# Optimization experiments

Hardware: AMD Instinct MI355X
Metric: run time of the kernel (lower is better)

Reference implementation:

```python
import jax, jax.numpy as jnp
import numpy as np

B, S, V, D, H, NL, FF, MAXD, OUTLEN, NC = 8, 1024, 64, 512, 8, 6, 2048, 64, 8, 10
HD = D // H


def _layernorm(x, g, b, eps=1e-5):
    m = jnp.mean(x, axis=-1, keepdims=True)
    v = jnp.var(x, axis=-1, keepdims=True)
    return (x - m) * jax.lax.rsqrt(v + eps) * g + b


def setup_inputs() -> dict:
    key = jax.random.key(0)
    ks = jax.random.split(key, 24)
    s = 0.02
    inp = {
        'src': jax.random.randint(ks[0], (B, S), 0, V, dtype=jnp.int32),
        'src_pad_mask': jnp.zeros((B, S), dtype=bool),
        'embed': jax.random.normal(ks[1], (V, D), jnp.float32) * s,
        'cls_token': jnp.zeros((D,), jnp.float32),
        'qkv_w': jax.random.normal(ks[2], (NL, 3 * D, D), jnp.float32) * s,
        'qkv_b': jnp.zeros((NL, 3 * D), jnp.float32),
        'out_w': jax.random.normal(ks[3], (NL, D, D), jnp.float32) * s,
        'out_b': jnp.zeros((NL, D), jnp.float32),
        'rel_emb': jax.random.normal(ks[4], (NL, 2 * MAXD + 1, H), jnp.float32) * s,
        'ln1_g': jnp.ones((NL, D), jnp.float32),
        'ln1_b': jnp.zeros((NL, D), jnp.float32),
        'w1': jax.random.normal(ks[5], (NL, FF, D), jnp.float32) * s,
        'b1': jnp.zeros((NL, FF), jnp.float32),
        'w2': jax.random.normal(ks[6], (NL, D, FF), jnp.float32) * s,
        'b2': jnp.zeros((NL, D), jnp.float32),
        'ln2_g': jnp.ones((NL, D), jnp.float32),
        'ln2_b': jnp.zeros((NL, D), jnp.float32),
        'norm_g': jnp.ones((D,), jnp.float32),
        'norm_b': jnp.zeros((D,), jnp.float32),
        'cls_w': jax.random.normal(ks[7], (OUTLEN * NC, D), jnp.float32) * s,
        'cls_b': jnp.zeros((OUTLEN * NC,), jnp.float32),
    }
    return inp


def _forward(src, src_pad_mask, embed, cls_token, qkv_w, qkv_b, out_w, out_b,
             rel_emb, ln1_g, ln1_b, w1, b1, w2, b2, ln2_g, ln2_b,
             norm_g, norm_b, cls_w, cls_b):
    b = src.shape[0]
    x = embed[src]                                         # [B,S,D]
    cls = jnp.broadcast_to(cls_token, (b, 1, D))
    x = jnp.concatenate([cls, x], axis=1)                  # [B,L,D], L=S+1
    L = x.shape[1]
    full_mask = jnp.concatenate([jnp.zeros((b, 1), bool), src_pad_mask], axis=1)

    # relative position indices, shared across layers
    rel = jnp.arange(L)[None, :] - jnp.arange(L)[:, None]  # [L,L]
    maxd = (rel_emb.shape[1] - 1) // 2
    rel = jnp.clip(rel, -maxd, maxd) + maxd
    scale = HD ** -0.5
    neg = jnp.asarray(-1e9, x.dtype)

    def layer(x, p):
        (qw, qb, ow, ob, re, g1, be1, W1, B1, W2, B2, g2, be2) = p
        qkv = jnp.einsum('bld,ed->ble', x, qw) + qb        # [B,L,3D]
        q, k, v = jnp.split(qkv, 3, axis=-1)
        q = q.reshape(b, L, H, HD)
        k = k.reshape(b, L, H, HD)
        v = v.reshape(b, L, H, HD)
        scores = jnp.einsum('bqhd,bkhd->bhqk', q, k) * scale
        bias = re[rel]                                     # [L,L,H]
        scores = scores + jnp.transpose(bias, (2, 0, 1))[None]
        scores = jnp.where(full_mask[:, None, None, :], neg, scores)
        attn = jax.nn.softmax(scores, axis=-1)
        o = jnp.einsum('bhqk,bkhd->bqhd', attn, v).reshape(b, L, D)
        o = jnp.einsum('bld,ed->ble', o, ow) + ob
        x2 = _layernorm(x + o, g1, be1)
        h = jax.nn.gelu(jnp.einsum('bld,fd->blf', x2, W1) + B1, approximate=False)
        ff = jnp.einsum('blf,df->bld', h, W2) + B2
        x3 = _layernorm(x2 + ff, g2, be2)
        return x3, None

    xs = (qkv_w, qkv_b, out_w, out_b, rel_emb, ln1_g, ln1_b,
          w1, b1, w2, b2, ln2_g, ln2_b)
    x, _ = jax.lax.scan(layer, x, xs)
    x = _layernorm(x, norm_g, norm_b)
    cls_repr = x[:, 0, :]
    logits = jnp.einsum('bd,od->bo', cls_repr, cls_w) + cls_b
    return logits.reshape(b, OUTLEN, NC)


def reference(src, src_pad_mask, embed, cls_token, qkv_w, qkv_b, out_w, out_b,
              rel_emb, ln1_g, ln1_b, w1, b1, w2, b2, ln2_g, ln2_b,
              norm_g, norm_b, cls_w, cls_b):
    return _forward(src, src_pad_mask, embed, cls_token, qkv_w, qkv_b, out_w,
                    out_b, rel_emb, ln1_g, ln1_b, w1, b1, w2, b2, ln2_g,
                    ln2_b, norm_g, norm_b, cls_w, cls_b)
```

## Files before the change

### kernel.cpp

```cpp
#include <hip/hip_runtime.h>
#include <hip/hip_bf16.h>
#include <stdint.h>

#define B 8
#define S 1024
#define L 1025
#define D 512
#define H 8
#define HD 64
#define NL 6
#define FF 2048
#define MAXD 64
#define OUTLEN 8
#define NC 10

#define MP 8320

typedef __bf16 bf16;
typedef __bf16 bf16x8 __attribute__((ext_vector_type(8)));
typedef __bf16 bf16x4 __attribute__((ext_vector_type(4)));
typedef float f32x4 __attribute__((ext_vector_type(4)));

__device__ __forceinline__ void gld16(const void* g, void* l) {
    __builtin_amdgcn_global_load_lds(
        (const __attribute__((address_space(1))) unsigned int*)g,
        (__attribute__((address_space(3))) unsigned int*)l,
        16, 0, 0);
}

__global__ __launch_bounds__(256) void cvt_k(const float* __restrict__ in,
                                             bf16* __restrict__ out, int n4)
{
    int i = blockIdx.x * 256 + threadIdx.x;
    if (i >= n4) return;
    float4 v = reinterpret_cast<const float4*>(in)[i];
    bf16x4 o;
    o[0] = (bf16)v.x; o[1] = (bf16)v.y; o[2] = (bf16)v.z; o[3] = (bf16)v.w;
    reinterpret_cast<bf16x4*>(out)[i] = o;
}

__global__ void embed_k(const int* __restrict__ src, const float* __restrict__ emb,
                        const float* __restrict__ cls, float* __restrict__ x,
                        bf16* __restrict__ xb)
{
    long i = (long)blockIdx.x * blockDim.x + threadIdx.x;
    if (i >= (long)B * L * D) return;
    int d = (int)(i % D);
    long bl = i / D;
    int l = (int)(bl % L);
    int b = (int)(bl / L);
    float v = (l == 0) ? cls[d] : emb[(long)src[b * S + (l - 1)] * D + d];
    x[i] = v;
    xb[i] = (bf16)v;
}

template<int ACT, int OBF>
__global__ __launch_bounds__(256) void mgemm(const bf16* __restrict__ A,
                                             const bf16* __restrict__ W,
                                             const float* __restrict__ bias,
                                             float* __restrict__ Cf,
                                             bf16* __restrict__ Cb,
                                             int N, int K)
{
    __shared__ bf16 Asl[128 * 32];
    __shared__ bf16 Bsl[128 * 32];
    int tid = threadIdx.x;
    int m0 = blockIdx.y * 128;
    int n0 = blockIdx.x * 128;
    int lane = tid & 63;
    int w = tid >> 6, wr = w >> 1, wc = w & 1;
    int wbase = tid & ~63;
    int kb = (lane >> 4) * 8;
    int rsel = lane & 15;
    f32x4 acc[4][4] = {};

    for (int k0 = 0; k0 < K; k0 += 32) {
#pragma unroll
        for (int r = 0; r < 2; r++) {
            int s = r * 256 + tid;
            int sb = r * 256 + wbase;
            gld16(A + (size_t)(m0 + (s >> 2)) * K + k0 + (s & 3) * 8, &Asl[(size_t)sb * 8]);
            gld16(W + (size_t)(n0 + (s >> 2)) * K + k0 + (s & 3) * 8, &Bsl[(size_t)sb * 8]);
        }
        __syncthreads();
        bf16x8 af[4], bfr[4];
#pragma unroll
        for (int fi = 0; fi < 4; fi++)
            af[fi] = *reinterpret_cast<const bf16x8*>(&Asl[(wr * 64 + fi * 16 + rsel) * 32 + kb]);
#pragma unroll
        for (int fj = 0; fj < 4; fj++)
            bfr[fj] = *reinterpret_cast<const bf16x8*>(&Bsl[(wc * 64 + fj * 16 + rsel) * 32 + kb]);
#pragma unroll
        for (int fi = 0; fi < 4; fi++)
#pragma unroll
            for (int fj = 0; fj < 4; fj++)
                acc[fi][fj] = __builtin_amdgcn_mfma_f32_16x16x32_bf16(af[fi], bfr[fj], acc[fi][fj], 0, 0, 0);
        __syncthreads();
    }
    int rowb = (lane >> 4) * 4;
    int colb = lane & 15;
#pragma unroll
    for (int fi = 0; fi < 4; fi++) {
#pragma unroll
        for (int fj = 0; fj < 4; fj++) {
            int col = n0 + wc * 64 + fj * 16 + colb;
            float bsv = bias[col];
#pragma unroll
            for (int i = 0; i < 4; i++) {
                int row = m0 + wr * 64 + fi * 16 + rowb + i;
                float v = acc[fi][fj][i] + bsv;
                if (ACT) v = 0.5f * v * (1.f + erff(v * 0.70710678118654752f));
                if (OBF) Cb[(size_t)row * N + col] = (bf16)v;
                else     Cf[(size_t)row * N + col] = v;
            }
        }
    }
}

__global__ __launch_bounds__(256) void fattn_k(const bf16* __restrict__ qkv,
                                               const float* __restrict__ rel_emb_l,
                                               const unsigned char* __restrict__ pad,
                                               bf16* __restrict__ ob)
{
    constexpr int PIT = 72;
    int qt = blockIdx.x, h = blockIdx.y, b = blockIdx.z;
    int q0 = qt * 64;
    __shared__ bf16 Qs[64 * PIT];
    __shared__ bf16 Ks[64 * PIT];
    __shared__ bf16 Vt[64 * PIT];
    __shared__ float bias_s[2 * MAXD + 1];
    __shared__ float msk_s[64];
    bf16* Ps = Qs;
    int tid = threadIdx.x;
    int lane = tid & 63;
    int w = tid >> 6;
    int ln15 = lane & 15;
    int g4 = lane >> 4;
    int kb8 = g4 * 8;
    const size_t bbase = (size_t)b * L * (3 * D) + (size_t)h * HD;

#pragma unroll
    for (int it = 0; it < 2; it++) {
        int s = tid + it * 256;
        int r = s >> 3, d0 = (s & 7) * 8;
        *(bf16x8*)(&Qs[r * PIT + d0]) =
            *(const bf16x8*)(qkv + bbase + (size_t)(q0 + r) * (3 * D) + d0);
    }
    for (int i = tid; i < 2 * MAXD + 1; i += 256) bias_s[i] = rel_emb_l[i * H + h];
    __syncthreads();

    bf16x8 qa0 = *(const bf16x8*)(&Qs[(w * 16 + ln15) * PIT + kb8]);
    bf16x8 qa1 = *(const bf16x8*)(&Qs[(w * 16 + ln15) * PIT + 32 + kb8]);

    f32x4 oacc[4] = {};
    float m_prev[4], l_sum[4];
#pragma unroll
    for (int i = 0; i < 4; i++) { m_prev[i] = -1e30f; l_sum[i] = 0.f; }

    for (int kt = 0; kt < 17; kt++) {
        int k0 = kt * 64;
        __syncthreads();
#pragma unroll
        for (int it = 0; it < 2; it++) {
            int s = tid + it * 256;
            int r = s >> 3, d0 = (s & 7) * 8;
            const bf16* rp = qkv + bbase + (size_t)(k0 + r) * (3 * D);
            bf16x8 kv = *(const bf16x8*)(rp + D + d0);
            bf16x8 vv = *(const bf16x8*)(rp + 2 * D + d0);
            *(bf16x8*)(&Ks[r * PIT + d0]) = kv;
            int ksw = r ^ ((s & 7) << 3);
#pragma unroll
            for (int j = 0; j < 8; j++)
                Vt[(d0 + j) * PIT + ksw] = vv[j];
        }
        if (tid < 64) {
            int gk = k0 + tid;
            msk_s[tid] = (gk >= L || (gk > 0 && pad[(size_t)b * S + gk - 1])) ? -1e9f : 0.f;
        }
        __syncthreads();

        f32x4 sacc[4] = {};
#pragma unroll
        for (int fj = 0; fj < 4; fj++) {
            bf16x8 kf0 = *(const bf16x8*)(&Ks[(fj * 16 + ln15) * PIT + kb8]);
            bf16x8 kf1 = *(const bf16x8*)(&Ks[(fj * 16 + ln15) * PIT + 32 + kb8]);
            sacc[fj] = __builtin_amdgcn_mfma_f32_16x16x32_bf16(qa0, kf0, sacc[fj], 0, 0, 0);
            sacc[fj] = __builtin_amdgcn_mfma_f32_16x16x32_bf16(qa1, kf1, sacc[fj], 0, 0, 0);
        }
        int rbase = q0 + w * 16 + g4 * 4;
        float sv[4][4];
#pragma unroll
        for (int fj = 0; fj < 4; fj++) {
            int cg = k0 + fj * 16 + ln15;
            float mv = msk_s[fj * 16 + ln15];
#pragma unroll
            for (int i = 0; i < 4; i++) {
                int rel = cg - (rbase + i);
                rel = min(MAXD, max(-MAXD, rel)) + MAXD;
                sv[fj][i] = sacc[fj][i] * 0.125f + bias_s[rel] + mv;
            }
        }
        float pb[4][4];
#pragma unroll
        for (int i = 0; i < 4; i++) {
            float mx = fmaxf(fmaxf(sv[0][i], sv[1][i]), fmaxf(sv[2][i], sv[3][i]));
#pragma unroll
            for (int msk = 1; msk < 16; msk <<= 1) mx = fmaxf(mx, __shfl_xor(mx, msk, 16));
            float mnew = fmaxf(m_prev[i], mx);
            float corr = __expf(m_prev[i] - mnew);
            float sum = 0.f;
#pragma unroll
            for (int fj = 0; fj < 4; fj++) {
                float p = __expf(sv[fj][i] - mnew);
                pb[fj][i] = p;
                sum += p;
            }
#pragma unroll
            for (int msk = 1; msk < 16; msk <<= 1) sum += __shfl_xor(sum, msk, 16);
            l_sum[i] = l_sum[i] * corr + sum;
            m_prev[i] = mnew;
#pragma unroll
            for (int fd = 0; fd < 4; fd++) oacc[fd][i] *= corr;
        }
#pragma unroll
        for (int i = 0; i < 4; i++) {
            int r = w * 16 + g4 * 4 + i;
            int cx = ((r >> 2) & 7) << 3;
#pragma unroll
            for (int fj = 0; fj < 4; fj++)
                Ps[r * PIT + ((fj * 16 + ln15) ^ cx)] = (bf16)pb[fj][i];
        }
        __syncthreads();
        int arow = w * 16 + ln15;
        int ax = ((arow >> 2) & 7) << 3;
        bf16x8 pa0 = *(const bf16x8*)(&Ps[arow * PIT + (kb8 ^ ax)]);
        bf16x8 pa1 = *(const bf16x8*)(&Ps[arow * PIT + ((32 + kb8) ^ ax)]);
#pragma unroll
        for (int fd = 0; fd < 4; fd++) {
            int d = fd * 16 + ln15;
            int vx = ((d >> 3) & 7) << 3;
            bf16x8 vf0 = *(const bf16x8*)(&Vt[d * PIT + (kb8 ^ vx)]);
            bf16x8 vf1 = *(const bf16x8*)(&Vt[d * PIT + ((32 + kb8) ^ vx)]);
            oacc[fd] = __builtin_amdgcn_mfma_f32_16x16x32_bf16(pa0, vf0, oacc[fd], 0, 0, 0);
            oacc[fd] = __builtin_amdgcn_mfma_f32_16x16x32_bf16(pa1, vf1, oacc[fd], 0, 0, 0);
        }
    }
#pragma unroll
    for (int i = 0; i < 4; i++) {
        int rg = q0 + w * 16 + g4 * 4 + i;
        if (rg >= L) continue;
        float inv = 1.f / l_sum[i];
#pragma unroll
        for (int fd = 0; fd < 4; fd++)
            ob[(size_t)(b * L + rg) * D + h * HD + fd * 16 + ln15] = (bf16)(oacc[fd][i] * inv);
    }
}

__global__ __launch_bounds__(256) void add_ln_k(const float* __restrict__ xin,
                                                const float* __restrict__ rin,
                                                const float* __restrict__ g,
                                                const float* __restrict__ bb,
                                                float* __restrict__ out,
                                                bf16* __restrict__ outb)
{
    int row = blockIdx.x;
    __shared__ float red[8];
    int tid = threadIdx.x;
    const float* xp = xin + (size_t)row * D;
    const float* rp = rin + (size_t)row * D;
    float v0 = xp[tid] + rp[tid];
    float v1 = xp[tid + 256] + rp[tid + 256];
    float s = v0 + v1;
    for (int off = 32; off; off >>= 1) s += __shfl_down(s, off, 64);
    int lane = tid & 63, wid = tid >> 6;
    if (lane == 0) red[wid] = s;
    __syncthreads();
    if (tid == 0) red[0] = red[0] + red[1] + red[2] + red[3];
    __syncthreads();
    float mean = red[0] * (1.f / D);
    float d0 = v0 - mean, d1 = v1 - mean;
    float sq = d0 * d0 + d1 * d1;
    for (int off = 32; off; off >>= 1) sq += __shfl_down(sq, off, 64);
    if (lane == 0) red[4 + wid] = sq;
    __syncthreads();
    if (tid == 0) red[4] = red[4] + red[5] + red[6] + red[7];
    __syncthreads();
    float rs = rsqrtf(red[4] * (1.f / D) + 1e-5f);
    float r0 = d0 * rs * g[tid] + bb[tid];
    float r1 = d1 * rs * g[tid + 256] + bb[tid + 256];
    out[(size_t)row * D + tid] = r0;
    out[(size_t)row * D + tid + 256] = r1;
    outb[(size_t)row * D + tid] = (bf16)r0;
    outb[(size_t)row * D + tid + 256] = (bf16)r1;
}

__global__ __launch_bounds__(256) void cls_k(const float* __restrict__ x,
                                             const float* __restrict__ ng,
                                             const float* __restrict__ nb,
                                             const float* __restrict__ cw,
                                             const float* __restrict__ cb,
                                             float* __restrict__ out)
{
    int b = blockIdx.x;
    __shared__ float xn[D];
    __shared__ float red[8];
    int tid = threadIdx.x;
    const float* xp = x + (size_t)(b * L) * D;
    float v0 = xp[tid], v1 = xp[tid + 256];
    float s = v0 + v1;
    for (int off = 32; off; off >>= 1) s += __shfl_down(s, off, 64);
    int lane = tid & 63, wid = tid >> 6;
    if (lane == 0) red[wid] = s;
    __syncthreads();
    if (tid == 0) red[0] = red[0] + red[1] + red[2] + red[3];
    __syncthreads();
    float mean = red[0] * (1.f / D);
    float d0 = v0 - mean, d1 = v1 - mean;
    float sq = d0 * d0 + d1 * d1;
    for (int off = 32; off; off >>= 1) sq += __shfl_down(sq, off, 64);
    if (lane == 0) red[4 + wid] = sq;
    __syncthreads();
    if (tid == 0) red[4] = red[4] + red[5] + red[6] + red[7];
    __syncthreads();
    float rs = rsqrtf(red[4] * (1.f / D) + 1e-5f);
    xn[tid] = d0 * rs * ng[tid] + nb[tid];
    xn[tid + 256] = d1 * rs * ng[tid + 256] + nb[tid + 256];
    __syncthreads();
    for (int o = tid; o < OUTLEN * NC; o += 256) {
        float acc = cb[o];
        const float* wp = cw + (size_t)o * D;
        for (int d = 0; d < D; d++) acc += xn[d] * wp[d];
        out[b * OUTLEN * NC + o] = acc;
    }
}

extern "C" void kernel_launch(void* const* d_in, const int* in_sizes, int n_in,
                              void* d_out, int out_size, void* d_ws, size_t ws_size,
                              hipStream_t stream) {
    const int* src = (const int*)d_in[0];
    const unsigned char* pad = (const unsigned char*)d_in[1];
    const float* emb = (const float*)d_in[2];
    const float* cls_token = (const float*)d_in[3];
    const float* qkv_w = (const float*)d_in[4];
    const float* qkv_b = (const float*)d_in[5];
    const float* out_w = (const float*)d_in[6];
    const float* out_b = (const float*)d_in[7];
    const float* rel_emb = (const float*)d_in[8];
    const float* ln1_g = (const float*)d_in[9];
    const float* ln1_b = (const float*)d_in[10];
    const float* w1 = (const float*)d_in[11];
    const float* b1 = (const float*)d_in[12];
    const float* w2 = (const float*)d_in[13];
    const float* b2 = (const float*)d_in[14];
    const float* ln2_g = (const float*)d_in[15];
    const float* ln2_b = (const float*)d_in[16];
    const float* norm_g = (const float*)d_in[17];
    const float* norm_b = (const float*)d_in[18];
    const float* cls_w = (const float*)d_in[19];
    const float* cls_b = (const float*)d_in[20];
    float* out = (float*)d_out;

    char* ws = (char*)d_ws;
    size_t off = 0;
    float* x   = (float*)(ws + off); off += (size_t)MP * D * 4;
    bf16*  xb  = (bf16*) (ws + off); off += (size_t)MP * D * 2;
    float* x2  = (float*)(ws + off); off += (size_t)MP * D * 4;
    bf16*  x2b = (bf16*) (ws + off); off += (size_t)MP * D * 2;
    char*  R   = ws + off;           off += (size_t)MP * 3 * D * 4;
    bf16*  qkvb = (bf16*)R;
    bf16*  hb  = (bf16*)R;
    float* p   = (float*)(R + (size_t)MP * FF * 2);
    bf16*  obf = (bf16*) (ws + off); off += (size_t)MP * D * 2;

    const size_t WQ = (size_t)NL * 3 * D * D;
    const size_t WO = (size_t)NL * D * D;
    const size_t W1E = (size_t)NL * FF * D;
    const size_t W2E = (size_t)NL * D * FF;
    const size_t WALL = WQ + WO + W1E + W2E;
    bool all_w = (off + WALL * 2) <= ws_size;

    bf16 *wq_a = nullptr, *wo_a = nullptr, *w1_a = nullptr, *w2_a = nullptr, *wbuf = nullptr;
    if (all_w) {
        wq_a = (bf16*)(ws + off);
        wo_a = wq_a + WQ;
        w1_a = wo_a + WO;
        w2_a = w1_a + W1E;
        int n4;
        n4 = (int)(WQ / 4);  cvt_k<<<dim3((n4 + 255) / 256), 256, 0, stream>>>(qkv_w, wq_a, n4);
        n4 = (int)(WO / 4);  cvt_k<<<dim3((n4 + 255) / 256), 256, 0, stream>>>(out_w, wo_a, n4);
        n4 = (int)(W1E / 4); cvt_k<<<dim3((n4 + 255) / 256), 256, 0, stream>>>(w1, w1_a, n4);
        n4 = (int)(W2E / 4); cvt_k<<<dim3((n4 + 255) / 256), 256, 0, stream>>>(w2, w2_a, n4);
    } else {
        wbuf = (bf16*)(ws + off);
    }

    const int M = B * L;
    {
        long total = (long)B * L * D;
        embed_k<<<dim3((unsigned)((total + 255) / 256)), 256, 0, stream>>>(src, emb, cls_token, x, xb);
    }
    for (int l = 0; l < NL; l++) {
        const float* qb  = qkv_b + (size_t)l * 3 * D;
        const float* obi = out_b + (size_t)l * D;
        const float* re  = rel_emb + (size_t)l * (2 * MAXD + 1) * H;
        const float* g1  = ln1_g + (size_t)l * D;
        const float* be1 = ln1_b + (size_t)l * D;
        const float* B1p = b1 + (size_t)l * FF;
        const float* B2p = b2 + (size_t)l * D;
        const float* g2  = ln2_g + (size_t)l * D;
        const float* be2 = ln2_b + (size_t)l * D;

        const bf16 *wqb, *wob, *w1b, *w2b;
        if (all_w) {
            wqb = wq_a + (size_t)l * 3 * D * D;
            wob = wo_a + (size_t)l * D * D;
            w1b = w1_a + (size_t)l * FF * D;
            w2b = w2_a + (size_t)l * D * FF;
        } else {
            bf16* wp_ = wbuf;
            wqb = wp_;            wp_ += 3 * D * D;
            wob = wp_;            wp_ += D * D;
            w1b = wp_;            wp_ += FF * D;
            w2b = wp_;
            int n4;
            n4 = 3 * D * D / 4; cvt_k<<<dim3((n4 + 255) / 256), 256, 0, stream>>>(qkv_w + (size_t)l * 3 * D * D, (bf16*)wqb, n4);
            n4 = D * D / 4;     cvt_k<<<dim3((n4 + 255) / 256), 256, 0, stream>>>(out_w + (size_t)l * D * D, (bf16*)wob, n4);
            n4 = FF * D / 4;    cvt_k<<<dim3((n4 + 255) / 256), 256, 0, stream>>>(w1 + (size_t)l * FF * D, (bf16*)w1b, n4);
            n4 = D * FF / 4;    cvt_k<<<dim3((n4 + 255) / 256), 256, 0, stream>>>(w2 + (size_t)l * D * FF, (bf16*)w2b, n4);
        }

        mgemm<0, 1><<<dim3(3 * D / 128, MP / 128), 256, 0, stream>>>(xb, wqb, qb, nullptr, qkvb, 3 * D, D);
        fattn_k<<<dim3((L + 63) / 64, H, B), 256, 0, stream>>>(qkvb, re, pad, obf);
        mgemm<0, 0><<<dim3(D / 128, MP / 128), 256, 0, stream>>>(obf, wob, obi, p, nullptr, D, D);
        add_ln_k<<<dim3(M), 256, 0, stream>>>(x, p, g1, be1, x2, x2b);
        mgemm<1, 1><<<dim3(FF / 128, MP / 128), 256, 0, stream>>>(x2b, w1b, B1p, nullptr, hb, FF, D);
        mgemm<0, 0><<<dim3(D / 128, MP / 128), 256, 0, stream>>>(hb, w2b, B2p, p, nullptr, D, FF);
        add_ln_k<<<dim3(M), 256, 0, stream>>>(x2, p, g2, be2, x, xb);
    }
    cls_k<<<dim3(B), 256, 0, stream>>>(x, norm_g, norm_b, cls_w, cls_b, out);
}
```

Measured before the change: 1.589 ms.

## Restructure flash attention with register K prefetch, double-buffered V, transposed MFMA

Rewrites the attention kernel so K fragments are read straight from global memory into registers and prefetched one tile ahead, while V is double-buffered in shared memory. The MFMA operands are swapped so each lane owns a single query row, which replaces the per-row 16-lane shuffle reductions with two shuffles. The softmax moves to exp2 with the scale and bias pre-multiplied by log2(e), and the bias gather is skipped for tiles lying entirely outside the relative-distance window. The aim is to overlap global loads with compute and cut shared-memory traffic and softmax ALU work, at the cost of more registers and a more intricate indexing scheme.

```diff
diff --git a/kernel.cpp b/kernel.cpp
--- a/kernel.cpp
+++ b/kernel.cpp
@@ -21,6 +21,8 @@
 typedef __bf16 bf16x4 __attribute__((ext_vector_type(4)));
 typedef float f32x4 __attribute__((ext_vector_type(4)));
 
+__device__ __forceinline__ float fexp2(float x) { return __builtin_amdgcn_exp2f(x); }
+
 __device__ __forceinline__ void gld16(const void* g, void* l) {
     __builtin_amdgcn_global_load_lds(
         (const __attribute__((address_space(1))) unsigned int*)g,
@@ -123,136 +125,172 @@
                                                bf16* __restrict__ ob)
 {
     constexpr int PIT = 72;
-    int qt = blockIdx.x, h = blockIdx.y, b = blockIdx.z;
-    int q0 = qt * 64;
-    __shared__ bf16 Qs[64 * PIT];
-    __shared__ bf16 Ks[64 * PIT];
-    __shared__ bf16 Vt[64 * PIT];
-    __shared__ float bias_s[2 * MAXD + 1];
-    __shared__ float msk_s[64];
-    bf16* Ps = Qs;
-    int tid = threadIdx.x;
-    int lane = tid & 63;
-    int w = tid >> 6;
-    int ln15 = lane & 15;
-    int g4 = lane >> 4;
-    int kb8 = g4 * 8;
-    const size_t bbase = (size_t)b * L * (3 * D) + (size_t)h * HD;
-
-#pragma unroll
-    for (int it = 0; it < 2; it++) {
-        int s = tid + it * 256;
-        int r = s >> 3, d0 = (s & 7) * 8;
-        *(bf16x8*)(&Qs[r * PIT + d0]) =
-            *(const bf16x8*)(qkv + bbase + (size_t)(q0 + r) * (3 * D) + d0);
-    }
-    for (int i = tid; i < 2 * MAXD + 1; i += 256) bias_s[i] = rel_emb_l[i * H + h];
-    __syncthreads();
-
-    bf16x8 qa0 = *(const bf16x8*)(&Qs[(w * 16 + ln15) * PIT + kb8]);
-    bf16x8 qa1 = *(const bf16x8*)(&Qs[(w * 16 + ln15) * PIT + 32 + kb8]);
+    __shared__ bf16 Vt[2][64 * PIT];
+    __shared__ bf16 Psh[4][16 * PIT];
+    __shared__ float bias2s[2 * MAXD + 1];
+    __shared__ float colm[2][64];
+
+    const int qt = blockIdx.x, h = blockIdx.y, b = blockIdx.z;
+    const int q0 = qt * 64;
+    const int tid = threadIdx.x;
+    const int lane = tid & 63;
+    const int w = tid >> 6;
+    const int ln15 = lane & 15, g4 = lane >> 4;
+    const int kb8 = g4 * 8;
+    constexpr float LOG2E = 1.4426950408889634f;
+    constexpr float C2 = 0.125f * LOG2E;
+
+    const char* base = (const char*)qkv + (size_t)(b * L) * 3072 + (size_t)h * (HD * 2);
+
+    for (int i = tid; i < 2 * MAXD + 1; i += 256) bias2s[i] = rel_emb_l[i * H + h] * LOG2E;
+    if (tid < 64) colm[0][tid] = (tid > 0 && pad[(size_t)b * S + tid - 1]) ? -1e9f : 0.f;
+
+    const int qrow = q0 + w * 16 + ln15;
+    bf16x8 qa0 = *(const bf16x8*)(base + (size_t)qrow * 3072 + g4 * 16);
+    bf16x8 qa1 = *(const bf16x8*)(base + (size_t)qrow * 3072 + 64 + g4 * 16);
+
+    const int vr = tid >> 3;
+    const int vd0 = (tid & 7) * 8;
+    const int vsw = ((vd0 >> 3) & 7) << 3;
+
+    {
+        bf16x8 a = *(const bf16x8*)(base + (size_t)vr * 3072 + 2048 + vd0 * 2);
+        bf16x8 c = *(const bf16x8*)(base + (size_t)(vr + 32) * 3072 + 2048 + vd0 * 2);
+#pragma unroll
+        for (int j = 0; j < 8; j++) {
+            Vt[0][(vd0 + j) * PIT + (vr ^ vsw)] = a[j];
+            Vt[0][(vd0 + j) * PIT + ((vr + 32) ^ vsw)] = c[j];
+        }
+    }
+    bf16x8 kr[4][2];
+#pragma unroll
+    for (int fj = 0; fj < 4; fj++) {
+        const char* rp = base + (size_t)(fj * 16 + ln15) * 3072 + 1024 + g4 * 16;
+        kr[fj][0] = *(const bf16x8*)(rp);
+        kr[fj][1] = *(const bf16x8*)(rp + 64);
+    }
+    __syncthreads();
 
     f32x4 oacc[4] = {};
-    float m_prev[4], l_sum[4];
-#pragma unroll
-    for (int i = 0; i < 4; i++) { m_prev[i] = -1e30f; l_sum[i] = 0.f; }
-
-    for (int kt = 0; kt < 17; kt++) {
-        int k0 = kt * 64;
+    float m_prev = -1e30f, l_sum = 0.f;
+
+    for (int t = 0; t < 17; t++) {
+        const int k0 = t * 64;
+        const int k0n = (k0 + 64 > 1024) ? 1024 : (k0 + 64);
+        const int cur = t & 1;
+
+        bf16x8 vA = *(const bf16x8*)(base + (size_t)(k0n + vr) * 3072 + 2048 + vd0 * 2);
+        bf16x8 vB = *(const bf16x8*)(base + (size_t)(k0n + vr + 32) * 3072 + 2048 + vd0 * 2);
+
+        f32x4 sacc[4] = {};
+#pragma unroll
+        for (int fj = 0; fj < 4; fj++) {
+            sacc[fj] = __builtin_amdgcn_mfma_f32_16x16x32_bf16(kr[fj][0], qa0, sacc[fj], 0, 0, 0);
+            sacc[fj] = __builtin_amdgcn_mfma_f32_16x16x32_bf16(kr[fj][1], qa1, sacc[fj], 0, 0, 0);
+        }
+#pragma unroll
+        for (int fj = 0; fj < 4; fj++) {
+            const char* rp = base + (size_t)(k0n + fj * 16 + ln15) * 3072 + 1024 + g4 * 16;
+            kr[fj][0] = *(const bf16x8*)(rp);
+            kr[fj][1] = *(const bf16x8*)(rp + 64);
+        }
+
+        float sv[4][4];
+        const int relbw = k0 - q0 - w * 16;
+        if (relbw >= MAXD + 15 || relbw <= -MAXD - 63) {
+            const float bu = bias2s[relbw > 0 ? 2 * MAXD : 0];
+#pragma unroll
+            for (int fj = 0; fj < 4; fj++) {
+                f32x4 cm = *(const f32x4*)&colm[cur][fj * 16 + g4 * 4];
+#pragma unroll
+                for (int i = 0; i < 4; i++)
+                    sv[fj][i] = fmaf(sacc[fj][i], C2, bu + cm[i]);
+            }
+        } else {
+            const int relb = k0 - qrow;
+#pragma unroll
+            for (int fj = 0; fj < 4; fj++) {
+                f32x4 cm = *(const f32x4*)&colm[cur][fj * 16 + g4 * 4];
+#pragma unroll
+                for (int i = 0; i < 4; i++) {
+                    int rel = relb + fj * 16 + g4 * 4 + i;
+                    rel = rel < -MAXD ? -MAXD : (rel > MAXD ? MAXD : rel);
+                    sv[fj][i] = fmaf(sacc[fj][i], C2, bias2s[rel + MAXD] + cm[i]);
+                }
+            }
+        }
+
+        float mx = sv[0][0];
+#pragma unroll
+        for (int fj = 0; fj < 4; fj++)
+#pragma unroll
+            for (int i = 0; i < 4; i++) mx = fmaxf(mx, sv[fj][i]);
+        mx = fmaxf(mx, __shfl_xor(mx, 16));
+        mx = fmaxf(mx, __shfl_xor(mx, 32));
+        const float mnew = fmaxf(m_prev, mx);
+        const float corr = fexp2(m_prev - mnew);
+        float pb[4][4];
+        float rsum = 0.f;
+#pragma unroll
+        for (int fj = 0; fj < 4; fj++)
+#pragma unroll
+            for (int i = 0; i < 4; i++) {
+                float p = fexp2(sv[fj][i] - mnew);
+                pb[fj][i] = p;
+                rsum += p;
+            }
+        rsum += __shfl_xor(rsum, 16);
+        rsum += __shfl_xor(rsum, 32);
+        l_sum = l_sum * corr + rsum;
+        m_prev = mnew;
+#pragma unroll
+        for (int fd = 0; fd < 4; fd++) oacc[fd] *= corr;
+
+#pragma unroll
+        for (int fj = 0; fj < 4; fj++) {
+            union { bf16 hh[4]; unsigned long long u; } pk;
+            pk.hh[0] = (bf16)pb[fj][0]; pk.hh[1] = (bf16)pb[fj][1];
+            pk.hh[2] = (bf16)pb[fj][2]; pk.hh[3] = (bf16)pb[fj][3];
+            *(unsigned long long*)&Psh[w][ln15 * PIT + fj * 16 + g4 * 4] = pk.u;
+        }
+
+#pragma unroll
+        for (int j = 0; j < 8; j++) {
+            Vt[cur ^ 1][(vd0 + j) * PIT + (vr ^ vsw)] = vA[j];
+            Vt[cur ^ 1][(vd0 + j) * PIT + ((vr + 32) ^ vsw)] = vB[j];
+        }
+        if (tid < 64) {
+            int gk = k0 + 64 + tid;
+            int pi = (gk <= 1024) ? gk - 1 : 0;
+            colm[cur ^ 1][tid] = (gk > 1024 || pad[(size_t)b * S + pi]) ? -1e9f : 0.f;
+        }
+
         __syncthreads();
-#pragma unroll
-        for (int it = 0; it < 2; it++) {
-            int s = tid + it * 256;
-            int r = s >> 3, d0 = (s & 7) * 8;
-            const bf16* rp = qkv + bbase + (size_t)(k0 + r) * (3 * D);
-            bf16x8 kv = *(const bf16x8*)(rp + D + d0);
-            bf16x8 vv = *(const bf16x8*)(rp + 2 * D + d0);
-            *(bf16x8*)(&Ks[r * PIT + d0]) = kv;
-            int ksw = r ^ ((s & 7) << 3);
-#pragma unroll
-            for (int j = 0; j < 8; j++)
-                Vt[(d0 + j) * PIT + ksw] = vv[j];
-        }
-        if (tid < 64) {
-            int gk = k0 + tid;
-            msk_s[tid] = (gk >= L || (gk > 0 && pad[(size_t)b * S + gk - 1])) ? -1e9f : 0.f;
+
+        bf16x8 pa0 = *(const bf16x8*)&Psh[w][ln15 * PIT + kb8];
+        bf16x8 pa1 = *(const bf16x8*)&Psh[w][ln15 * PIT + 32 + kb8];
+#pragma unroll
+        for (int fd = 0; fd < 4; fd++) {
+            const int d = fd * 16 + ln15;
+            const int vx = ((d >> 3) & 7) << 3;
+            bf16x8 af0 = *(const bf16x8*)&Vt[cur][d * PIT + (kb8 ^ vx)];
+            bf16x8 af1 = *(const bf16x8*)&Vt[cur][d * PIT + ((32 + kb8) ^ vx)];
+            oacc[fd] = __builtin_amdgcn_mfma_f32_16x16x32_bf16(af0, pa0, oacc[fd], 0, 0, 0);
+            oacc[fd] = __builtin_amdgcn_mfma_f32_16x16x32_bf16(af1, pa1, oacc[fd], 0, 0, 0);
         }
         __syncthreads();
-
-        f32x4 sacc[4] = {};
-#pragma unroll
-        for (int fj = 0; fj < 4; fj++) {
-            bf16x8 kf0 = *(const bf16x8*)(&Ks[(fj * 16 + ln15) * PIT + kb8]);
-            bf16x8 kf1 = *(const bf16x8*)(&Ks[(fj * 16 + ln15) * PIT + 32 + kb8]);
-            sacc[fj] = __builtin_amdgcn_mfma_f32_16x16x32_bf16(qa0, kf0, sacc[fj], 0, 0, 0);
-            sacc[fj] = __builtin_amdgcn_mfma_f32_16x16x32_bf16(qa1, kf1, sacc[fj], 0, 0, 0);
-        }
-        int rbase = q0 + w * 16 + g4 * 4;
-        float sv[4][4];
-#pragma unroll
-        for (int fj = 0; fj < 4; fj++) {
-            int cg = k0 + fj * 16 + ln15;
-            float mv = msk_s[fj * 16 + ln15];
-#pragma unroll
-            for (int i = 0; i < 4; i++) {
-                int rel = cg - (rbase + i);
-                rel = min(MAXD, max(-MAXD, rel)) + MAXD;
-                sv[fj][i] = sacc[fj][i] * 0.125f + bias_s[rel] + mv;
-            }
-        }
-        float pb[4][4];
-#pragma unroll
-        for (int i = 0; i < 4; i++) {
-            float mx = fmaxf(fmaxf(sv[0][i], sv[1][i]), fmaxf(sv[2][i], sv[3][i]));
-#pragma unroll
-            for (int msk = 1; msk < 16; msk <<= 1) mx = fmaxf(mx, __shfl_xor(mx, msk, 16));
-            float mnew = fmaxf(m_prev[i], mx);
-            float corr = __expf(m_prev[i] - mnew);
-            float sum = 0.f;
-#pragma unroll
-            for (int fj = 0; fj < 4; fj++) {
-                float p = __expf(sv[fj][i] - mnew);
-                pb[fj][i] = p;
-                sum += p;
-            }
-#pragma unroll
-            for (int msk = 1; msk < 16; msk <<= 1) sum += __shfl_xor(sum, msk, 16);
-            l_sum[i] = l_sum[i] * corr + sum;
-            m_prev[i] = mnew;
-#pragma unroll
-            for (int fd = 0; fd < 4; fd++) oacc[fd][i] *= corr;
-        }
-#pragma unroll
-        for (int i = 0; i < 4; i++) {
-            int r = w * 16 + g4 * 4 + i;
-            int cx = ((r >> 2) & 7) << 3;
-#pragma unroll
-            for (int fj = 0; fj < 4; fj++)
-                Ps[r * PIT + ((fj * 16 + ln15) ^ cx)] = (bf16)pb[fj][i];
-        }
-        __syncthreads();
-        int arow = w * 16 + ln15;
-        int ax = ((arow >> 2) & 7) << 3;
-        bf16x8 pa0 = *(const bf16x8*)(&Ps[arow * PIT + (kb8 ^ ax)]);
-        bf16x8 pa1 = *(const bf16x8*)(&Ps[arow * PIT + ((32 + kb8) ^ ax)]);
+    }
+
+    if (qrow < L) {
+        const float inv = 1.f / l_sum;
+        bf16* op = ob + (size_t)(b * L + qrow) * D + h * HD + g4 * 4;
 #pragma unroll
         for (int fd = 0; fd < 4; fd++) {
-            int d = fd * 16 + ln15;
-            int vx = ((d >> 3) & 7) << 3;
-            bf16x8 vf0 = *(const bf16x8*)(&Vt[d * PIT + (kb8 ^ vx)]);
-            bf16x8 vf1 = *(const bf16x8*)(&Vt[d * PIT + ((32 + kb8) ^ vx)]);
-            oacc[fd] = __builtin_amdgcn_mfma_f32_16x16x32_bf16(pa0, vf0, oacc[fd], 0, 0, 0);
-            oacc[fd] = __builtin_amdgcn_mfma_f32_16x16x32_bf16(pa1, vf1, oacc[fd], 0, 0, 0);
-        }
-    }
-#pragma unroll
-    for (int i = 0; i < 4; i++) {
-        int rg = q0 + w * 16 + g4 * 4 + i;
-        if (rg >= L) continue;
-        float inv = 1.f / l_sum[i];
-#pragma unroll
-        for (int fd = 0; fd < 4; fd++)
-            ob[(size_t)(b * L + rg) * D + h * HD + fd * 16 + ln15] = (bf16)(oacc[fd][i] * inv);
+            bf16x4 r;
+#pragma unroll
+            for (int i = 0; i < 4; i++) r[i] = (bf16)(oacc[fd][i] * inv);
+            *(bf16x4*)(op + fd * 16) = r;
+        }
     }
 }
 
```

After: 1.590 ms. No clear change (+0.1%).
